# Optimization experiments

Hardware: AMD Instinct MI355X
Metric: run time of the kernel (lower is better)

The kernel has to match this reference:

```python
import jax, jax.numpy as jnp
import numpy as np

NUM_USER = 100000
NUM_ITEM = 50000
N_NODES = NUM_USER + NUM_ITEM
EMBED_DIM = 64
ALGEBRA_DIM = 4
NUM_LAYERS = 2
DIM_FEAT = 512
N_EDGES_DIR = 500000  # undirected interactions; doubled to 1M directed edges


def _xavier_uniform(key, shape):
    bound = np.sqrt(6.0 / (shape[0] + shape[1]))
    return jax.random.uniform(key, shape, minval=-bound, maxval=bound, dtype=jnp.float32)


def setup_inputs() -> dict:
    key = jax.random.key(0)
    ks = jax.random.split(key, 8)
    emb_s = _xavier_uniform(ks[0], (NUM_USER, EMBED_DIM))
    # algebra_dim-1 extra user component embeddings, stacked [A-1, num_user, D]
    emb_x = jnp.stack([_xavier_uniform(jax.random.fold_in(ks[1], i), (NUM_USER, EMBED_DIM))
                       for i in range(ALGEBRA_DIM - 1)])
    # xavier_normal for prompt_emb [N, A*D]
    std = np.sqrt(2.0 / (N_NODES + EMBED_DIM * ALGEBRA_DIM))
    prompt_emb = jax.random.normal(ks[2], (N_NODES, EMBED_DIM * ALGEBRA_DIM), dtype=jnp.float32) * std
    mlp_w = _xavier_uniform(ks[3], (DIM_FEAT, 4 * EMBED_DIM))
    mlp_b = jnp.zeros((4 * EMBED_DIM,), jnp.float32)
    mlp1_w = _xavier_uniform(ks[4], (4 * EMBED_DIM, EMBED_DIM))
    mlp1_b = jnp.zeros((EMBED_DIM,), jnp.float32)
    features = jax.random.normal(ks[5], (NUM_ITEM, DIM_FEAT), dtype=jnp.float32)
    # bipartite user<->item edges, symmetric, no self loops by construction
    u = jax.random.randint(ks[6], (N_EDGES_DIR,), 0, NUM_USER)
    it = jax.random.randint(ks[7], (N_EDGES_DIR,), NUM_USER, N_NODES)
    edge_index = jnp.stack([jnp.concatenate([u, it]), jnp.concatenate([it, u])]).astype(jnp.int32)
    return {"edge_index": edge_index, "features": features, "emb_s": emb_s, "emb_x": emb_x,
            "prompt_emb": prompt_emb, "mlp_w": mlp_w, "mlp_b": mlp_b,
            "mlp1_w": mlp1_w, "mlp1_b": mlp1_b}


def _l2norm(x):  # F.normalize(x, dim=1)
    return x / jnp.maximum(jnp.linalg.norm(x, axis=1, keepdims=True), 1e-12)


def reference(edge_index, features, emb_s, emb_x, prompt_emb, mlp_w, mlp_b, mlp1_w, mlp1_b):
    row, col = edge_index[0], edge_index[1]
    # item feature projection: MLP_1(leaky_relu(MLP(features)))
    temp = jax.nn.leaky_relu(features @ mlp_w + mlp_b, 0.01) @ mlp1_w + mlp1_b  # [num_item, D]
    # algebra components: each is L2-normalized cat(user_emb, item_feat) -> [N, D]
    comps = [_l2norm(jnp.concatenate([emb_s, temp], axis=0))]
    for i in range(ALGEBRA_DIM - 1):
        comps.append(_l2norm(jnp.concatenate([emb_x[i], temp], axis=0)))
    # symmetric GCN normalization; deg computed over source (row) indices
    deg = jax.ops.segment_sum(jnp.ones(row.shape, jnp.float32), row, num_segments=N_NODES)
    dinv = deg ** -0.5  # inf only at never-indexed nodes (unused)
    norm = (dinv[row] * dinv[col])[:, None]  # [E, 1]
    total = None
    for _ in range(NUM_LAYERS):
        # propagate each component: out[col] += norm * x[row]
        comps = [jax.ops.segment_sum(norm * c[row], col, num_segments=N_NODES) for c in comps]
        layer_out = jnp.concatenate(comps, axis=1)  # [N, A*D]
        total = layer_out if total is None else total + layer_out
    combined = total + prompt_emb
    return combined
```

## Files before the change

kernel.cpp:

```cpp
#include <hip/hip_runtime.h>
#include <hip/hip_bf16.h>

#define NUM_USER 100000
#define NUM_ITEM 50000
#define N_NODES  150000
#define EMBED_DIM 64
#define ALG 4
#define DIM_FEAT 512
#define NEDGE 1000000

__global__ __launch_bounds__(256) void count_kernel(const int* __restrict__ row, int* __restrict__ deg)
{
    int e = blockIdx.x * 256 + threadIdx.x;
    if (e < NEDGE) atomicAdd(&deg[row[e]], 1);
}

__global__ __launch_bounds__(1024) void scan_kernel(const int* __restrict__ deg, int* __restrict__ off, int n)
{
    __shared__ int wpart[17];
    const int tid = threadIdx.x;
    const int lane = tid & 63, w = tid >> 6;
    int running = 0;
    for (int base = 0; base < n; base += 1024) {
        int i = base + tid;
        int v = (i < n) ? deg[i] : 0;
        int x = v;
        #pragma unroll
        for (int d = 1; d < 64; d <<= 1) {
            int t = __shfl_up(x, d);
            if (lane >= d) x += t;
        }
        if (lane == 63) wpart[w] = x;
        __syncthreads();
        if (tid == 0) {
            int a = 0;
            #pragma unroll
            for (int j = 0; j < 16; ++j) { int t = wpart[j]; wpart[j] = a; a += t; }
            wpart[16] = a;
        }
        __syncthreads();
        if (i < n) off[i] = running + wpart[w] + (x - v);
        running += wpart[16];
        __syncthreads();
    }
    if (tid == 0) off[n] = running;
}

__global__ __launch_bounds__(256) void dinv_kernel(const int* __restrict__ deg, float* __restrict__ dinv)
{
    int n = blockIdx.x * 256 + threadIdx.x;
    if (n < N_NODES) {
        int d = deg[n];
        dinv[n] = d > 0 ? 1.0f / sqrtf((float)d) : 0.0f;
    }
}

__global__ __launch_bounds__(256) void fill_kernel(const int* __restrict__ row, const int* __restrict__ col,
                                                   const int* __restrict__ off, int* __restrict__ cursor,
                                                   const float* __restrict__ dinv,
                                                   int* __restrict__ csr_src, float* __restrict__ csr_nrm)
{
    int e = blockIdx.x * 256 + threadIdx.x;
    if (e < NEDGE) {
        int r = row[e], c = col[e];
        int p = atomicAdd(&cursor[c], 1);
        int idx = off[c] + p;
        csr_src[idx] = r;
        csr_nrm[idx] = dinv[r] * dinv[c];
    }
}

__global__ __launch_bounds__(256) void gemm1_kernel(const float* __restrict__ A, const float* __restrict__ B,
                                                    const float* __restrict__ bias, float* __restrict__ C)
{
    __shared__ float As[16][132];
    __shared__ float Bs[16][128];
    const int tid = threadIdx.x;
    const int tx = tid & 15, ty = tid >> 4;
    const int m0 = blockIdx.x * 128, n0 = blockIdx.y * 128;
    float acc[8][8] = {};
    for (int k0 = 0; k0 < 512; k0 += 16) {
        #pragma unroll
        for (int rep = 0; rep < 2; ++rep) {
            int idx = tid + rep * 256;
            int m = idx >> 2;
            int kc = (idx & 3) << 2;
            int row = m0 + m;
            float4 v = make_float4(0.f, 0.f, 0.f, 0.f);
            if (row < 50000) v = *(const float4*)&A[(size_t)row * 512 + k0 + kc];
            As[kc + 0][m] = v.x; As[kc + 1][m] = v.y; As[kc + 2][m] = v.z; As[kc + 3][m] = v.w;
        }
        #pragma unroll
        for (int rep = 0; rep < 2; ++rep) {
            int idx = tid + rep * 256;
            int kk = idx >> 5;
            int nc = (idx & 31) << 2;
            float4 v = *(const float4*)&B[(size_t)(k0 + kk) * 256 + n0 + nc];
            *(float4*)&Bs[kk][nc] = v;
        }
        __syncthreads();
        #pragma unroll
        for (int k = 0; k < 16; ++k) {
            float4 a0 = *(const float4*)&As[k][ty * 8];
            float4 a1 = *(const float4*)&As[k][ty * 8 + 4];
            float4 b0 = *(const float4*)&Bs[k][tx * 8];
            float4 b1 = *(const float4*)&Bs[k][tx * 8 + 4];
            float a[8] = {a0.x, a0.y, a0.z, a0.w, a1.x, a1.y, a1.z, a1.w};
            float b[8] = {b0.x, b0.y, b0.z, b0.w, b1.x, b1.y, b1.z, b1.w};
            #pragma unroll
            for (int i = 0; i < 8; ++i)
                #pragma unroll
                for (int j = 0; j < 8; ++j)
                    acc[i][j] += a[i] * b[j];
        }
        __syncthreads();
    }
    float4 bv0 = *(const float4*)&bias[n0 + tx * 8];
    float4 bv1 = *(const float4*)&bias[n0 + tx * 8 + 4];
    float bb[8] = {bv0.x, bv0.y, bv0.z, bv0.w, bv1.x, bv1.y, bv1.z, bv1.w};
    #pragma unroll
    for (int i = 0; i < 8; ++i) {
        int row = m0 + ty * 8 + i;
        if (row < 50000) {
            float o[8];
            #pragma unroll
            for (int j = 0; j < 8; ++j) {
                float t = acc[i][j] + bb[j];
                o[j] = t >= 0.f ? t : 0.01f * t;
            }
            *(float4*)&C[(size_t)row * 256 + n0 + tx * 8]     = make_float4(o[0], o[1], o[2], o[3]);
            *(float4*)&C[(size_t)row * 256 + n0 + tx * 8 + 4] = make_float4(o[4], o[5], o[6], o[7]);
        }
    }
}

__global__ __launch_bounds__(256) void gemm2_kernel(const float* __restrict__ A, const float* __restrict__ B,
                                                    const float* __restrict__ bias, float* __restrict__ C)
{
    __shared__ float As[16][132];
    __shared__ float Bs[16][64];
    const int tid = threadIdx.x;
    const int tx = tid & 15, ty = tid >> 4;
    const int m0 = blockIdx.x * 128;
    float acc[8][4] = {};
    for (int k0 = 0; k0 < 256; k0 += 16) {
        #pragma unroll
        for (int rep = 0; rep < 2; ++rep) {
            int idx = tid + rep * 256;
            int m = idx >> 2;
            int kc = (idx & 3) << 2;
            int row = m0 + m;
            float4 v = make_float4(0.f, 0.f, 0.f, 0.f);
            if (row < 50000) v = *(const float4*)&A[(size_t)row * 256 + k0 + kc];
            As[kc + 0][m] = v.x; As[kc + 1][m] = v.y; As[kc + 2][m] = v.z; As[kc + 3][m] = v.w;
        }
        {
            int kk = tid >> 4;
            int nc = (tid & 15) << 2;
            float4 v = *(const float4*)&B[(size_t)(k0 + kk) * 64 + nc];
            *(float4*)&Bs[kk][nc] = v;
        }
        __syncthreads();
        #pragma unroll
        for (int k = 0; k < 16; ++k) {
            float4 a0 = *(const float4*)&As[k][ty * 8];
            float4 a1 = *(const float4*)&As[k][ty * 8 + 4];
            float4 b0 = *(const float4*)&Bs[k][tx * 4];
            float a[8] = {a0.x, a0.y, a0.z, a0.w, a1.x, a1.y, a1.z, a1.w};
            float b[4] = {b0.x, b0.y, b0.z, b0.w};
            #pragma unroll
            for (int i = 0; i < 8; ++i)
                #pragma unroll
                for (int j = 0; j < 4; ++j)
                    acc[i][j] += a[i] * b[j];
        }
        __syncthreads();
    }
    float4 bv = *(const float4*)&bias[tx * 4];
    #pragma unroll
    for (int i = 0; i < 8; ++i) {
        int row = m0 + ty * 8 + i;
        if (row < 50000) {
            float4 o = make_float4(acc[i][0] + bv.x, acc[i][1] + bv.y, acc[i][2] + bv.z, acc[i][3] + bv.w);
            *(float4*)&C[(size_t)row * 64 + tx * 4] = o;
        }
    }
}

__global__ __launch_bounds__(256) void build_x0_kernel(const float* __restrict__ emb_s, const float* __restrict__ emb_x,
                                                       const float* __restrict__ temp, float* __restrict__ x0)
{
    int wid = (blockIdx.x * 256 + threadIdx.x) >> 6;
    int lane = threadIdx.x & 63;
    if (wid >= N_NODES) return;
    if (wid < NUM_USER) {
        #pragma unroll
        for (int a = 0; a < ALG; ++a) {
            const float* srcp = (a == 0) ? &emb_s[(size_t)wid * 64]
                                         : &emb_x[((size_t)(a - 1) * NUM_USER + wid) * 64];
            float v = srcp[lane];
            float ss = v * v;
            #pragma unroll
            for (int m = 1; m < 64; m <<= 1) ss += __shfl_xor(ss, m);
            float inv = 1.0f / fmaxf(sqrtf(ss), 1e-12f);
            x0[(size_t)wid * 256 + a * 64 + lane] = v * inv;
        }
    } else {
        float v = temp[(size_t)(wid - NUM_USER) * 64 + lane];
        float ss = v * v;
        #pragma unroll
        for (int m = 1; m < 64; m <<= 1) ss += __shfl_xor(ss, m);
        float inv = 1.0f / fmaxf(sqrtf(ss), 1e-12f);
        float r = v * inv;
        #pragma unroll
        for (int a = 0; a < ALG; ++a)
            x0[(size_t)wid * 256 + a * 64 + lane] = r;
    }
}

__global__ __launch_bounds__(256) void prop_kernel(const float4* __restrict__ xin, float4* __restrict__ xout,
                                                   const int* __restrict__ off, const int* __restrict__ src,
                                                   const float* __restrict__ nrm,
                                                   const float4* __restrict__ addA, const float4* __restrict__ addB)
{
    int wid = (blockIdx.x * 256 + threadIdx.x) >> 6;
    int lane = threadIdx.x & 63;
    if (wid >= N_NODES) return;
    int o0 = off[wid], o1 = off[wid + 1];
    float4 acc = make_float4(0.f, 0.f, 0.f, 0.f);
    int i = o0;
    for (; i + 1 < o1; i += 2) {
        int s0 = src[i], s1 = src[i + 1];
        float w0 = nrm[i], w1 = nrm[i + 1];
        float4 v0 = xin[(size_t)s0 * 64 + lane];
        float4 v1 = xin[(size_t)s1 * 64 + lane];
        acc.x += w0 * v0.x; acc.y += w0 * v0.y; acc.z += w0 * v0.z; acc.w += w0 * v0.w;
        acc.x += w1 * v1.x; acc.y += w1 * v1.y; acc.z += w1 * v1.z; acc.w += w1 * v1.w;
    }
    if (i < o1) {
        int s0 = src[i];
        float w0 = nrm[i];
        float4 v0 = xin[(size_t)s0 * 64 + lane];
        acc.x += w0 * v0.x; acc.y += w0 * v0.y; acc.z += w0 * v0.z; acc.w += w0 * v0.w;
    }
    size_t oi = (size_t)wid * 64 + lane;
    if (addA) {
        float4 a = addA[oi];
        float4 b = addB[oi];
        acc.x += a.x + b.x; acc.y += a.y + b.y; acc.z += a.z + b.z; acc.w += a.w + b.w;
    }
    xout[oi] = acc;
}

extern "C" void kernel_launch(void* const* d_in, const int* in_sizes, int n_in,
                              void* d_out, int out_size, void* d_ws, size_t ws_size,
                              hipStream_t stream)
{
    const int*   edge     = (const int*)d_in[0];
    const float* features = (const float*)d_in[1];
    const float* emb_s    = (const float*)d_in[2];
    const float* emb_x    = (const float*)d_in[3];
    const float* prompt   = (const float*)d_in[4];
    const float* mlp_w    = (const float*)d_in[5];
    const float* mlp_b    = (const float*)d_in[6];
    const float* mlp1_w   = (const float*)d_in[7];
    const float* mlp1_b   = (const float*)d_in[8];
    float*       out      = (float*)d_out;

    const int* row = edge;
    const int* col = edge + NEDGE;

    const size_t NX = (size_t)N_NODES * 256;
    float* ws     = (float*)d_ws;
    float* x0     = ws;
    float* x1     = ws + NX;
    float* temp1  = x1;
    float* temp   = x1 + (size_t)50000 * 256;
    int*   deg    = (int*)(ws + 2 * NX);
    int*   cursor = deg + 150016;
    int*   off    = cursor + 150016;
    int*   csr_src = off + 150016;
    float* csr_nrm = (float*)(csr_src + NEDGE);
    float* dinv    = csr_nrm + NEDGE;

    hipMemsetAsync(deg, 0, 2 * 150016 * sizeof(int), stream);

    count_kernel<<<(NEDGE + 255) / 256, 256, 0, stream>>>(row, deg);
    scan_kernel<<<1, 1024, 0, stream>>>(deg, off, N_NODES);
    dinv_kernel<<<(N_NODES + 255) / 256, 256, 0, stream>>>(deg, dinv);
    fill_kernel<<<(NEDGE + 255) / 256, 256, 0, stream>>>(row, col, off, cursor, dinv, csr_src, csr_nrm);

    gemm1_kernel<<<dim3(391, 2), 256, 0, stream>>>(features, mlp_w, mlp_b, temp1);
    gemm2_kernel<<<dim3(391, 1), 256, 0, stream>>>(temp1, mlp1_w, mlp1_b, temp);

    build_x0_kernel<<<N_NODES / 4, 256, 0, stream>>>(emb_s, emb_x, temp, x0);

    prop_kernel<<<N_NODES / 4, 256, 0, stream>>>((const float4*)x0, (float4*)x1,
                                                 off, csr_src, csr_nrm, nullptr, nullptr);
    prop_kernel<<<N_NODES / 4, 256, 0, stream>>>((const float4*)x1, (float4*)out,
                                                 off, csr_src, csr_nrm,
                                                 (const float4*)x1, (const float4*)prompt);
}
```

Baseline: 1.140 ms.

## Replace FP32 SIMT GEMMs with split-bf16 MFMA GEMMs

Replaces the two scalar FP32 tiled GEMMs of the item MLP with one templated MFMA kernel. Each FP32 value is split into high and low bf16 parts, and three bf16 MFMAs per tile (hh, hl, lh) recover near-FP32 accuracy. A prep kernel transposes and splits the weights into scratch space that x0 later reuses. The aim is to move GEMM arithmetic onto matrix cores, at the cost of splitting A on the fly, scalar output stores and slightly reduced precision.

After: 1.012 ms. -11.2%, faster.

```diff
diff --git a/kernel.cpp b/kernel.cpp
--- a/kernel.cpp
+++ b/kernel.cpp
@@ -8,6 +8,9 @@
 #define ALG 4
 #define DIM_FEAT 512
 #define NEDGE 1000000
+
+typedef __attribute__((ext_vector_type(8))) short bf16x8;
+typedef __attribute__((ext_vector_type(4))) float f32x4;
 
 __global__ __launch_bounds__(256) void count_kernel(const int* __restrict__ row, int* __restrict__ deg)
 {
@@ -70,119 +73,139 @@
     }
 }
 
-__global__ __launch_bounds__(256) void gemm1_kernel(const float* __restrict__ A, const float* __restrict__ B,
-                                                    const float* __restrict__ bias, float* __restrict__ C)
-{
-    __shared__ float As[16][132];
-    __shared__ float Bs[16][128];
-    const int tid = threadIdx.x;
-    const int tx = tid & 15, ty = tid >> 4;
-    const int m0 = blockIdx.x * 128, n0 = blockIdx.y * 128;
-    float acc[8][8] = {};
-    for (int k0 = 0; k0 < 512; k0 += 16) {
-        #pragma unroll
-        for (int rep = 0; rep < 2; ++rep) {
-            int idx = tid + rep * 256;
-            int m = idx >> 2;
-            int kc = (idx & 3) << 2;
-            int row = m0 + m;
-            float4 v = make_float4(0.f, 0.f, 0.f, 0.f);
-            if (row < 50000) v = *(const float4*)&A[(size_t)row * 512 + k0 + kc];
-            As[kc + 0][m] = v.x; As[kc + 1][m] = v.y; As[kc + 2][m] = v.z; As[kc + 3][m] = v.w;
-        }
-        #pragma unroll
-        for (int rep = 0; rep < 2; ++rep) {
-            int idx = tid + rep * 256;
-            int kk = idx >> 5;
-            int nc = (idx & 31) << 2;
-            float4 v = *(const float4*)&B[(size_t)(k0 + kk) * 256 + n0 + nc];
-            *(float4*)&Bs[kk][nc] = v;
-        }
-        __syncthreads();
-        #pragma unroll
-        for (int k = 0; k < 16; ++k) {
-            float4 a0 = *(const float4*)&As[k][ty * 8];
-            float4 a1 = *(const float4*)&As[k][ty * 8 + 4];
-            float4 b0 = *(const float4*)&Bs[k][tx * 8];
-            float4 b1 = *(const float4*)&Bs[k][tx * 8 + 4];
-            float a[8] = {a0.x, a0.y, a0.z, a0.w, a1.x, a1.y, a1.z, a1.w};
-            float b[8] = {b0.x, b0.y, b0.z, b0.w, b1.x, b1.y, b1.z, b1.w};
-            #pragma unroll
-            for (int i = 0; i < 8; ++i)
+__device__ __forceinline__ void split_bf16(float v, unsigned short& h, unsigned short& l)
+{
+    unsigned int u = __float_as_uint(v);
+    unsigned int hu = u & 0xFFFF0000u;
+    float lf = v - __uint_as_float(hu);
+    h = (unsigned short)(u >> 16);
+    l = (unsigned short)(__float_as_uint(lf) >> 16);
+}
+
+__global__ __launch_bounds__(256) void convert_b_kernel(const float* __restrict__ B1, const float* __restrict__ B2,
+                                                        unsigned short* __restrict__ Bt1h, unsigned short* __restrict__ Bt1l,
+                                                        unsigned short* __restrict__ Bt2h, unsigned short* __restrict__ Bt2l)
+{
+    int i = blockIdx.x * 256 + threadIdx.x;
+    if (i < 512 * 256) {
+        int k = i >> 8, n = i & 255;
+        unsigned short h, l;
+        split_bf16(B1[i], h, l);
+        Bt1h[n * 512 + k] = h;
+        Bt1l[n * 512 + k] = l;
+    } else {
+        int j = i - 512 * 256;
+        if (j < 256 * 64) {
+            int k = j >> 6, n = j & 63;
+            unsigned short h, l;
+            split_bf16(B2[j], h, l);
+            Bt2h[n * 256 + k] = h;
+            Bt2l[n * 256 + k] = l;
+        }
+    }
+}
+
+template<int M, int K, int N, int NF, bool LRELU>
+__global__ __launch_bounds__(256) void gemm_mfma_kernel(const float* __restrict__ A,
+                                                        const unsigned short* __restrict__ Bth,
+                                                        const unsigned short* __restrict__ Btl,
+                                                        const float* __restrict__ bias,
+                                                        float* __restrict__ C)
+{
+    constexpr int BN = NF * 32;
+    __shared__ unsigned short Ah[128][40], Al[128][40];
+    __shared__ unsigned short Bh[BN][40],  Bl[BN][40];
+
+    const int tid  = threadIdx.x;
+    const int lane = tid & 63;
+    const int wid  = tid >> 6;
+    const int wr = wid >> 1, wc = wid & 1;
+    const int fm = lane & 15;
+    const int fk = (lane >> 4) * 8;
+    const int m0 = blockIdx.x * 128;
+    const int n0 = blockIdx.y * BN;
+
+    const int sr = tid >> 1;
+    const int sh = tid & 1;
+
+    f32x4 acc[4][NF];
+    #pragma unroll
+    for (int i = 0; i < 4; ++i)
+        #pragma unroll
+        for (int j = 0; j < NF; ++j)
+            acc[i][j] = (f32x4){0.f, 0.f, 0.f, 0.f};
+
+    for (int k0 = 0; k0 < K; k0 += 32) {
+        {
+            int row = m0 + sr;
+            float va[16];
+            if (row < M) {
+                const float* ap = &A[(size_t)row * K + k0 + sh * 16];
                 #pragma unroll
-                for (int j = 0; j < 8; ++j)
-                    acc[i][j] += a[i] * b[j];
-        }
-        __syncthreads();
-    }
-    float4 bv0 = *(const float4*)&bias[n0 + tx * 8];
-    float4 bv1 = *(const float4*)&bias[n0 + tx * 8 + 4];
-    float bb[8] = {bv0.x, bv0.y, bv0.z, bv0.w, bv1.x, bv1.y, bv1.z, bv1.w};
+                for (int c = 0; c < 4; ++c) {
+                    float4 v = *(const float4*)&ap[c * 4];
+                    va[c * 4 + 0] = v.x; va[c * 4 + 1] = v.y; va[c * 4 + 2] = v.z; va[c * 4 + 3] = v.w;
+                }
+            } else {
+                #pragma unroll
+                for (int c = 0; c < 16; ++c) va[c] = 0.f;
+            }
+            union { unsigned short s[16]; float4 f[2]; } uh, ul;
+            #pragma unroll
+            for (int c = 0; c < 16; ++c) split_bf16(va[c], uh.s[c], ul.s[c]);
+            *(float4*)&Ah[sr][sh * 16]     = uh.f[0];
+            *(float4*)&Ah[sr][sh * 16 + 8] = uh.f[1];
+            *(float4*)&Al[sr][sh * 16]     = ul.f[0];
+            *(float4*)&Al[sr][sh * 16 + 8] = ul.f[1];
+        }
+        if (sr < BN) {
+            const unsigned short* bp = &Bth[(size_t)(n0 + sr) * K + k0 + sh * 16];
+            *(float4*)&Bh[sr][sh * 16]     = *(const float4*)&bp[0];
+            *(float4*)&Bh[sr][sh * 16 + 8] = *(const float4*)&bp[8];
+            const unsigned short* lp = &Btl[(size_t)(n0 + sr) * K + k0 + sh * 16];
+            *(float4*)&Bl[sr][sh * 16]     = *(const float4*)&lp[0];
+            *(float4*)&Bl[sr][sh * 16 + 8] = *(const float4*)&lp[8];
+        }
+        __syncthreads();
+
+        bf16x8 fah[4], fal[4], fbh[NF], fbl[NF];
+        #pragma unroll
+        for (int i = 0; i < 4; ++i) {
+            fah[i] = *(const bf16x8*)&Ah[wr * 64 + i * 16 + fm][fk];
+            fal[i] = *(const bf16x8*)&Al[wr * 64 + i * 16 + fm][fk];
+        }
+        #pragma unroll
+        for (int j = 0; j < NF; ++j) {
+            fbh[j] = *(const bf16x8*)&Bh[wc * NF * 16 + j * 16 + fm][fk];
+            fbl[j] = *(const bf16x8*)&Bl[wc * NF * 16 + j * 16 + fm][fk];
+        }
+        #pragma unroll
+        for (int i = 0; i < 4; ++i)
+            #pragma unroll
+            for (int j = 0; j < NF; ++j) {
+                acc[i][j] = __builtin_amdgcn_mfma_f32_16x16x32_bf16(fah[i], fbh[j], acc[i][j], 0, 0, 0);
+                acc[i][j] = __builtin_amdgcn_mfma_f32_16x16x32_bf16(fah[i], fbl[j], acc[i][j], 0, 0, 0);
+                acc[i][j] = __builtin_amdgcn_mfma_f32_16x16x32_bf16(fal[i], fbh[j], acc[i][j], 0, 0, 0);
+            }
+        __syncthreads();
+    }
+
     #pragma unroll
-    for (int i = 0; i < 8; ++i) {
-        int row = m0 + ty * 8 + i;
-        if (row < 50000) {
-            float o[8];
-            #pragma unroll
-            for (int j = 0; j < 8; ++j) {
-                float t = acc[i][j] + bb[j];
-                o[j] = t >= 0.f ? t : 0.01f * t;
+    for (int i = 0; i < 4; ++i) {
+        int rbase = m0 + wr * 64 + i * 16 + (lane >> 4) * 4;
+        #pragma unroll
+        for (int j = 0; j < NF; ++j) {
+            int col = n0 + wc * NF * 16 + j * 16 + fm;
+            float bv = bias[col];
+            #pragma unroll
+            for (int q = 0; q < 4; ++q) {
+                int r = rbase + q;
+                if (r < M) {
+                    float o = acc[i][j][q] + bv;
+                    if (LRELU) o = o >= 0.f ? o : 0.01f * o;
+                    C[(size_t)r * N + col] = o;
+                }
             }
-            *(float4*)&C[(size_t)row * 256 + n0 + tx * 8]     = make_float4(o[0], o[1], o[2], o[3]);
-            *(float4*)&C[(size_t)row * 256 + n0 + tx * 8 + 4] = make_float4(o[4], o[5], o[6], o[7]);
-        }
-    }
-}
-
-__global__ __launch_bounds__(256) void gemm2_kernel(const float* __restrict__ A, const float* __restrict__ B,
-                                                    const float* __restrict__ bias, float* __restrict__ C)
-{
-    __shared__ float As[16][132];
-    __shared__ float Bs[16][64];
-    const int tid = threadIdx.x;
-    const int tx = tid & 15, ty = tid >> 4;
-    const int m0 = blockIdx.x * 128;
-    float acc[8][4] = {};
-    for (int k0 = 0; k0 < 256; k0 += 16) {
-        #pragma unroll
-        for (int rep = 0; rep < 2; ++rep) {
-            int idx = tid + rep * 256;
-            int m = idx >> 2;
-            int kc = (idx & 3) << 2;
-            int row = m0 + m;
-            float4 v = make_float4(0.f, 0.f, 0.f, 0.f);
-            if (row < 50000) v = *(const float4*)&A[(size_t)row * 256 + k0 + kc];
-            As[kc + 0][m] = v.x; As[kc + 1][m] = v.y; As[kc + 2][m] = v.z; As[kc + 3][m] = v.w;
-        }
-        {
-            int kk = tid >> 4;
-            int nc = (tid & 15) << 2;
-            float4 v = *(const float4*)&B[(size_t)(k0 + kk) * 64 + nc];
-            *(float4*)&Bs[kk][nc] = v;
-        }
-        __syncthreads();
-        #pragma unroll
-        for (int k = 0; k < 16; ++k) {
-            float4 a0 = *(const float4*)&As[k][ty * 8];
-            float4 a1 = *(const float4*)&As[k][ty * 8 + 4];
-            float4 b0 = *(const float4*)&Bs[k][tx * 4];
-            float a[8] = {a0.x, a0.y, a0.z, a0.w, a1.x, a1.y, a1.z, a1.w};
-            float b[4] = {b0.x, b0.y, b0.z, b0.w};
-            #pragma unroll
-            for (int i = 0; i < 8; ++i)
-                #pragma unroll
-                for (int j = 0; j < 4; ++j)
-                    acc[i][j] += a[i] * b[j];
-        }
-        __syncthreads();
-    }
-    float4 bv = *(const float4*)&bias[tx * 4];
-    #pragma unroll
-    for (int i = 0; i < 8; ++i) {
-        int row = m0 + ty * 8 + i;
-        if (row < 50000) {
-            float4 o = make_float4(acc[i][0] + bv.x, acc[i][1] + bv.y, acc[i][2] + bv.z, acc[i][3] + bv.w);
-            *(float4*)&C[(size_t)row * 64 + tx * 4] = o;
         }
     }
 }
@@ -283,15 +306,22 @@
     float* csr_nrm = (float*)(csr_src + NEDGE);
     float* dinv    = csr_nrm + NEDGE;
 
+    unsigned short* Bt1h = (unsigned short*)x0;
+    unsigned short* Bt1l = Bt1h + 256 * 512;
+    unsigned short* Bt2h = Bt1l + 256 * 512;
+    unsigned short* Bt2l = Bt2h + 64 * 256;
+
     hipMemsetAsync(deg, 0, 2 * 150016 * sizeof(int), stream);
+
+    convert_b_kernel<<<576, 256, 0, stream>>>(mlp_w, mlp1_w, Bt1h, Bt1l, Bt2h, Bt2l);
 
     count_kernel<<<(NEDGE + 255) / 256, 256, 0, stream>>>(row, deg);
     scan_kernel<<<1, 1024, 0, stream>>>(deg, off, N_NODES);
     dinv_kernel<<<(N_NODES + 255) / 256, 256, 0, stream>>>(deg, dinv);
     fill_kernel<<<(NEDGE + 255) / 256, 256, 0, stream>>>(row, col, off, cursor, dinv, csr_src, csr_nrm);
 
-    gemm1_kernel<<<dim3(391, 2), 256, 0, stream>>>(features, mlp_w, mlp_b, temp1);
-    gemm2_kernel<<<dim3(391, 1), 256, 0, stream>>>(temp1, mlp1_w, mlp1_b, temp);
+    gemm_mfma_kernel<50000, 512, 256, 4, true ><<<dim3(391, 2), 256, 0, stream>>>(features, Bt1h, Bt1l, mlp_b, temp1);
+    gemm_mfma_kernel<50000, 256,  64, 2, false><<<dim3(391, 1), 256, 0, stream>>>(temp1,    Bt2h, Bt2l, mlp1_b, temp);
 
     build_x0_kernel<<<N_NODES / 4, 256, 0, stream>>>(emb_s, emb_x, temp, x0);
 
```
